# Performance work log

Measured on AMD Instinct MI355X. Metric: run time of the kernel, lower is better.

The kernel has to match this reference:

```python
import jax, jax.numpy as jnp
import numpy as np

N_NODES = 50000
N_EDGES = 800000
HIDDEN = 128          # hidden_dim
MSG = HIDDEN // 2     # message_dim = LSTM hidden size


def setup_inputs() -> dict:
    key = jax.random.key(0)
    ks = jax.random.split(key, 9)
    feat = jax.random.normal(ks[0], (N_NODES, HIDDEN), dtype=jnp.float32)
    src0 = jax.random.randint(ks[1], (N_EDGES,), 0, N_NODES, dtype=jnp.int32)
    dst0 = jax.random.randint(ks[2], (N_EDGES,), 0, N_NODES, dtype=jnp.int32)
    src1 = jax.random.randint(ks[3], (N_EDGES,), 0, N_NODES, dtype=jnp.int32)
    dst1 = jax.random.randint(ks[4], (N_EDGES,), 0, N_NODES, dtype=jnp.int32)
    # PyTorch LSTMCell params: gates order (i, f, g, o), scale 1/sqrt(hidden)
    s = 1.0 / np.sqrt(MSG)
    W_ih = jax.random.uniform(ks[5], (4 * MSG, HIDDEN), jnp.float32, -s, s)
    W_hh = jax.random.uniform(ks[6], (4 * MSG, MSG), jnp.float32, -s, s)
    b_ih = jax.random.uniform(ks[7], (4 * MSG,), jnp.float32, -s, s)
    b_hh = jax.random.uniform(ks[8], (4 * MSG,), jnp.float32, -s, s)
    return {"feat": feat, "src0": src0, "dst0": dst0, "src1": src1,
            "dst1": dst1, "W_ih": W_ih, "W_hh": W_hh, "b_ih": b_ih, "b_hh": b_hh}


def _etype_mean(feat, src, dst, n_nodes):
    """copy_u('h','m') + mean('m','ft') for one edge type."""
    m = feat[src]                                             # [E, H] gather
    s = jax.ops.segment_sum(m, dst, num_segments=n_nodes)    # [N, H]
    cnt = jax.ops.segment_sum(jnp.ones(src.shape, feat.dtype), dst,
                              num_segments=n_nodes)          # [N]
    mean = s / jnp.maximum(cnt, 1.0)[:, None]
    return mean, (cnt > 0).astype(feat.dtype)


def reference(feat, src0, dst0, src1, dst1, W_ih, W_hh, b_ih, b_hh):
    n = feat.shape[0]
    ft0, has0 = _etype_mean(feat, src0, dst0, n)
    ft1, has1 = _etype_mean(feat, src1, dst1, n)
    # cross_reducer='mean': average over etypes that delivered messages
    n_active = jnp.maximum(has0 + has1, 1.0)[:, None]
    rst = (ft0 + ft1) / n_active                              # [N, H]

    G_t = rst[:, :MSG]   # h0
    R_t = rst[:, MSG:]   # c0

    # PyTorch LSTMCell: gates = x W_ih^T + b_ih + h W_hh^T + b_hh
    gates = feat @ W_ih.T + b_ih + G_t @ W_hh.T + b_hh       # [N, 4*MSG]
    i, f, g, o = jnp.split(gates, 4, axis=1)
    c1 = jax.nn.sigmoid(f) * R_t + jax.nn.sigmoid(i) * jnp.tanh(g)
    h1 = jax.nn.sigmoid(o) * jnp.tanh(c1)
    return jnp.concatenate([h1, c1], axis=1)                  # [N, H]
```

## Files before the change

kernel.cpp:

```cpp
#include <hip/hip_runtime.h>
#include <hip/hip_fp16.h>
#include <cmath>

#define NN 50000
#define NE 800000
#define NPB 32
#define NBKT 196
#define BKT_SHIFT 8
#define BKT_NODES 256
#define BKT_CAP 6144
#define CHUNK 4096
#define NCH 196

using f16x8 = __attribute__((ext_vector_type(8))) _Float16;
using f32x4 = __attribute__((ext_vector_type(4))) float;

__device__ __forceinline__ float sigmoidf_(float x) {
    return 1.0f / (1.0f + __expf(-x));
}
__device__ __forceinline__ float tanhf_(float x) {
    float t = __expf(-2.0f * fabsf(x));
    float r = (1.0f - t) / (1.0f + t);
    return copysignf(r, x);
}

__global__ __launch_bounds__(256) void prep_kernel(
    const float* __restrict__ feat, __half* __restrict__ feat_h,
    const float* __restrict__ Wih, const float* __restrict__ Whh,
    const float* __restrict__ b_ih, const float* __restrict__ b_hh,
    __half* __restrict__ WC, float* __restrict__ bsum,
    int* __restrict__ bcnt) {
    int i = blockIdx.x * blockDim.x + threadIdx.x;

    {
        const float4 v = ((const float4*)feat)[i];
        __half2 lo = __floats2half2_rn(v.x, v.y);
        __half2 hi = __floats2half2_rn(v.z, v.w);
        ((__half2*)feat_h)[2 * i]     = lo;
        ((__half2*)feat_h)[2 * i + 1] = hi;
    }
    if (i < 256 * 128) {
        int g = i >> 7, k = i & 127;
        WC[(size_t)g * 192 + k] = __float2half(Wih[i]);
    }
    if (i < 256 * 64) {
        int g = i >> 6, k = i & 63;
        WC[(size_t)g * 192 + 128 + k] = __float2half(Whh[i]);
    }
    if (i < 256) bsum[i] = b_ih[i] + b_hh[i];
    if (i < 2 * NBKT) bcnt[i] = 0;
}

__global__ __launch_bounds__(256) void bin_kernel(
    const int* __restrict__ src0, const int* __restrict__ dst0,
    const int* __restrict__ src1, const int* __restrict__ dst1,
    int* __restrict__ bcnt,
    unsigned* __restrict__ binned0, unsigned* __restrict__ binned1) {
    __shared__ int cnt[NBKT];
    __shared__ int base[NBKT];
    __shared__ int cur[NBKT];
    __shared__ int sdst[CHUNK];

    int x  = blockIdx.x;
    int et = x >= NCH;
    int c  = et ? x - NCH : x;
    const int* src = et ? src1 : src0;
    const int* dst = et ? dst1 : dst0;
    unsigned* binned = et ? binned1 : binned0;

    int start = c * CHUNK;
    int n = min(CHUNK, NE - start);
    int tid = threadIdx.x;

    if (tid < NBKT) { cnt[tid] = 0; cur[tid] = 0; }
    __syncthreads();
    for (int i = tid; i < n; i += 256) {
        int d = dst[start + i];
        sdst[i] = d;
        atomicAdd(&cnt[d >> BKT_SHIFT], 1);
    }
    __syncthreads();
    if (tid < NBKT && cnt[tid] > 0)
        base[tid] = atomicAdd(&bcnt[et * NBKT + tid], cnt[tid]);
    __syncthreads();
    for (int i = tid; i < n; i += 256) {
        int d = sdst[i];
        int b = d >> BKT_SHIFT;
        int r = atomicAdd(&cur[b], 1);
        binned[(size_t)b * BKT_CAP + base[b] + r] =
            ((unsigned)d << 16) | (unsigned)src[start + i];
    }
}

__global__ __launch_bounds__(256) void bucket_scatter_kernel(
    const unsigned* __restrict__ binned0, const unsigned* __restrict__ binned1,
    const int* __restrict__ bcnt,
    int* __restrict__ off0, int* __restrict__ off1,
    int* __restrict__ deg0, int* __restrict__ deg1,
    unsigned short* __restrict__ es0, unsigned short* __restrict__ es1) {
    __shared__ int lcnt[BKT_NODES];
    __shared__ int lbase[BKT_NODES];

    int g  = blockIdx.x;
    int et = g >= NBKT;
    int b  = et ? g - NBKT : g;
    const unsigned* binned = (et ? binned1 : binned0) + (size_t)b * BKT_CAP;
    int* off = et ? off1 : off0;
    int* deg = et ? deg1 : deg0;
    unsigned short* es = (et ? es1 : es0) + (size_t)b * BKT_CAP;

    int bn = bcnt[g];
    int node0 = b * BKT_NODES;
    int tid = threadIdx.x;

    lcnt[tid] = 0;
    __syncthreads();
    for (int i = tid; i < bn; i += 256) {
        unsigned u = binned[i];
        int d = (int)(u >> 16) - node0;
        atomicAdd(&lcnt[d], 1);
    }
    __syncthreads();
    int cntv = lcnt[tid];
    for (int d = 1; d < BKT_NODES; d <<= 1) {
        int v = (tid >= d) ? lcnt[tid - d] : 0;
        __syncthreads();
        lcnt[tid] += v;
        __syncthreads();
    }
    int excl = lcnt[tid] - cntv;
    lbase[tid] = excl;
    int gn = node0 + tid;
    if (gn < NN) { off[gn] = b * BKT_CAP + excl; deg[gn] = cntv; }
    __syncthreads();
    for (int i = tid; i < bn; i += 256) {
        unsigned u = binned[i];
        int d = (int)(u >> 16) - node0;
        int r = atomicAdd(&lbase[d], 1);
        es[r] = (unsigned short)(u & 0xffffu);
    }
}

__global__ __launch_bounds__(256) void gather_kernel(
    const uint2* __restrict__ featu,
    const unsigned short* __restrict__ es0, const int* __restrict__ off0, const int* __restrict__ deg0,
    const unsigned short* __restrict__ es1, const int* __restrict__ off1, const int* __restrict__ deg1,
    uint2* __restrict__ rstu) {
    int wid  = (blockIdx.x * blockDim.x + threadIdx.x) >> 6;
    int lane = threadIdx.x & 63;
    if (wid >= NN) return;
    int hf = lane >> 5;
    int c  = lane & 31;

    float a0[4] = {0.f, 0.f, 0.f, 0.f};
    float a1[4] = {0.f, 0.f, 0.f, 0.f};

    int d0 = deg0[wid], o0 = off0[wid];
    int e = 0;
    for (; e + 8 <= d0; e += 8) {
        int s0 = es0[o0 + e + 0 + hf];
        int s1 = es0[o0 + e + 2 + hf];
        int s2 = es0[o0 + e + 4 + hf];
        int s3 = es0[o0 + e + 6 + hf];
        uint2 v0 = featu[(size_t)s0 * 32 + c];
        uint2 v1 = featu[(size_t)s1 * 32 + c];
        uint2 v2 = featu[(size_t)s2 * 32 + c];
        uint2 v3 = featu[(size_t)s3 * 32 + c];
#pragma unroll
        for (int k = 0; k < 1; k++) { }
        {
            float2 f;
            f = __half22float2(*(__half2*)&v0.x); a0[0] += f.x; a0[1] += f.y;
            f = __half22float2(*(__half2*)&v0.y); a0[2] += f.x; a0[3] += f.y;
            f = __half22float2(*(__half2*)&v1.x); a0[0] += f.x; a0[1] += f.y;
            f = __half22float2(*(__half2*)&v1.y); a0[2] += f.x; a0[3] += f.y;
            f = __half22float2(*(__half2*)&v2.x); a0[0] += f.x; a0[1] += f.y;
            f = __half22float2(*(__half2*)&v2.y); a0[2] += f.x; a0[3] += f.y;
            f = __half22float2(*(__half2*)&v3.x); a0[0] += f.x; a0[1] += f.y;
            f = __half22float2(*(__half2*)&v3.y); a0[2] += f.x; a0[3] += f.y;
        }
    }
    if (e < d0) {
        int last = d0 - 1;
#pragma unroll
        for (int j = 0; j < 4; j++) {
            int ee = e + 2 * j + hf;
            int s = es0[o0 + min(ee, last)];
            uint2 v = featu[(size_t)s * 32 + c];
            float m = (ee < d0) ? 1.f : 0.f;
            float2 f;
            f = __half22float2(*(__half2*)&v.x); a0[0] = fmaf(f.x, m, a0[0]); a0[1] = fmaf(f.y, m, a0[1]);
            f = __half22float2(*(__half2*)&v.y); a0[2] = fmaf(f.x, m, a0[2]); a0[3] = fmaf(f.y, m, a0[3]);
        }
    }

    int d1 = deg1[wid], o1 = off1[wid];
    e = 0;
    for (; e + 8 <= d1; e += 8) {
        int s0 = es1[o1 + e + 0 + hf];
        int s1 = es1[o1 + e + 2 + hf];
        int s2 = es1[o1 + e + 4 + hf];
        int s3 = es1[o1 + e + 6 + hf];
        uint2 v0 = featu[(size_t)s0 * 32 + c];
        uint2 v1 = featu[(size_t)s1 * 32 + c];
        uint2 v2 = featu[(size_t)s2 * 32 + c];
        uint2 v3 = featu[(size_t)s3 * 32 + c];
        {
            float2 f;
            f = __half22float2(*(__half2*)&v0.x); a1[0] += f.x; a1[1] += f.y;
            f = __half22float2(*(__half2*)&v0.y); a1[2] += f.x; a1[3] += f.y;
            f = __half22float2(*(__half2*)&v1.x); a1[0] += f.x; a1[1] += f.y;
            f = __half22float2(*(__half2*)&v1.y); a1[2] += f.x; a1[3] += f.y;
            f = __half22float2(*(__half2*)&v2.x); a1[0] += f.x; a1[1] += f.y;
            f = __half22float2(*(__half2*)&v2.y); a1[2] += f.x; a1[3] += f.y;
            f = __half22float2(*(__half2*)&v3.x); a1[0] += f.x; a1[1] += f.y;
            f = __half22float2(*(__half2*)&v3.y); a1[2] += f.x; a1[3] += f.y;
        }
    }
    if (e < d1) {
        int last = d1 - 1;
#pragma unroll
        for (int j = 0; j < 4; j++) {
            int ee = e + 2 * j + hf;
            int s = es1[o1 + min(ee, last)];
            uint2 v = featu[(size_t)s * 32 + c];
            float m = (ee < d1) ? 1.f : 0.f;
            float2 f;
            f = __half22float2(*(__half2*)&v.x); a1[0] = fmaf(f.x, m, a1[0]); a1[1] = fmaf(f.y, m, a1[1]);
            f = __half22float2(*(__half2*)&v.y); a1[2] = fmaf(f.x, m, a1[2]); a1[3] = fmaf(f.y, m, a1[3]);
        }
    }

#pragma unroll
    for (int k = 0; k < 4; k++) {
        a0[k] += __shfl_xor(a0[k], 32, 64);
        a1[k] += __shfl_xor(a1[k], 32, 64);
    }

    if (hf == 0) {
        float inv0 = 1.0f / fmaxf((float)d0, 1.0f);
        float inv1 = 1.0f / fmaxf((float)d1, 1.0f);
        float na = fmaxf((float)((d0 > 0) + (d1 > 0)), 1.0f);
        float r0 = (a0[0] * inv0 + a1[0] * inv1) / na;
        float r1 = (a0[1] * inv0 + a1[1] * inv1) / na;
        float r2 = (a0[2] * inv0 + a1[2] * inv1) / na;
        float r3 = (a0[3] * inv0 + a1[3] * inv1) / na;
        __half2 h01 = __floats2half2_rn(r0, r1);
        __half2 h23 = __floats2half2_rn(r2, r3);
        uint2 o;
        o.x = *(unsigned*)&h01;
        o.y = *(unsigned*)&h23;
        rstu[(size_t)wid * 32 + c] = o;
    }
}

__global__ __launch_bounds__(256) void node_kernel(
    const __half* __restrict__ feat_h,
    const __half* __restrict__ rst_h,
    const __half* __restrict__ WC, const float* __restrict__ bsum,
    float* __restrict__ out) {
    __shared__ __half xs[32 * 200];

    int t  = threadIdx.x;
    int nb = blockIdx.x * NPB;
    int lane = t & 63;
    int w    = t >> 6;
    int col  = lane & 15;
    int g4   = lane >> 4;

    f16x8 bfr[4][6];
    float bias[4];
#pragma unroll
    for (int ct = 0; ct < 4; ct++) {
        int gate = ct * 64 + w * 16 + col;
        bias[ct] = bsum[gate];
#pragma unroll
        for (int ks = 0; ks < 6; ks++)
            bfr[ct][ks] = *(const f16x8*)(WC + (size_t)gate * 192 + ks * 32 + g4 * 8);
    }

    const uint4* feat4 = (const uint4*)feat_h;
    const uint4* rst4  = (const uint4*)rst_h;
#pragma unroll
    for (int j = 0; j < 2; j++) {
        int e = t + j * 256;
        int n = e >> 4, q = e & 15;
        int gn = nb + n;
        uint4 v = make_uint4(0, 0, 0, 0);
        if (gn < NN) v = feat4[(size_t)gn * 16 + q];
        *(uint4*)(&xs[n * 200 + q * 8]) = v;
    }
    {
        int n = t >> 3, q = t & 7;
        int gn = nb + n;
        uint4 v = make_uint4(0, 0, 0, 0);
        if (gn < NN) v = rst4[(size_t)gn * 16 + q];
        *(uint4*)(&xs[n * 200 + 128 + q * 8]) = v;
    }
    __syncthreads();

    f32x4 acc[2][4];
#pragma unroll
    for (int rt = 0; rt < 2; rt++)
#pragma unroll
        for (int ct = 0; ct < 4; ct++)
            acc[rt][ct] = (f32x4){bias[ct], bias[ct], bias[ct], bias[ct]};

#pragma unroll
    for (int ks = 0; ks < 6; ks++) {
        f16x8 a0 = *(const f16x8*)(&xs[(col) * 200 + ks * 32 + g4 * 8]);
        f16x8 a1 = *(const f16x8*)(&xs[(16 + col) * 200 + ks * 32 + g4 * 8]);
#pragma unroll
        for (int ct = 0; ct < 4; ct++) {
            acc[0][ct] = __builtin_amdgcn_mfma_f32_16x16x32_f16(a0, bfr[ct][ks], acc[0][ct], 0, 0, 0);
            acc[1][ct] = __builtin_amdgcn_mfma_f32_16x16x32_f16(a1, bfr[ct][ks], acc[1][ct], 0, 0, 0);
        }
    }

    int m = w * 16 + col;
#pragma unroll
    for (int rt = 0; rt < 2; rt++) {
#pragma unroll
        for (int r = 0; r < 4; r++) {
            int nl = rt * 16 + g4 * 4 + r;
            int gn = nb + nl;
            if (gn >= NN) continue;
            float iv = sigmoidf_(acc[rt][0][r]);
            float fv = sigmoidf_(acc[rt][1][r]);
            float gv = tanhf_(acc[rt][2][r]);
            float ov = sigmoidf_(acc[rt][3][r]);
            float R  = __half2float(rst_h[(size_t)gn * 128 + 64 + m]);
            float c1 = fv * R + iv * gv;
            float h1 = ov * tanhf_(c1);
            out[(size_t)gn * 128 + m]      = h1;
            out[(size_t)gn * 128 + 64 + m] = c1;
        }
    }
}

extern "C" void kernel_launch(void* const* d_in, const int* in_sizes, int n_in,
                              void* d_out, int out_size, void* d_ws, size_t ws_size,
                              hipStream_t stream) {
    const float* feat = (const float*)d_in[0];
    const int*   src0 = (const int*)d_in[1];
    const int*   dst0 = (const int*)d_in[2];
    const int*   src1 = (const int*)d_in[3];
    const int*   dst1 = (const int*)d_in[4];
    const float* W_ih = (const float*)d_in[5];
    const float* W_hh = (const float*)d_in[6];
    const float* b_ih = (const float*)d_in[7];
    const float* b_hh = (const float*)d_in[8];
    float* out = (float*)d_out;

    char* p = (char*)d_ws;
    int* bcnt = (int*)p;            p += 2 * NBKT * 4;
    int* off0 = (int*)p;            p += NN * 4;
    int* off1 = (int*)p;            p += NN * 4;
    int* deg0 = (int*)p;            p += NN * 4;
    int* deg1 = (int*)p;            p += NN * 4;
    unsigned* binned0 = (unsigned*)p; p += (size_t)NBKT * BKT_CAP * 4;
    unsigned* binned1 = (unsigned*)p; p += (size_t)NBKT * BKT_CAP * 4;
    unsigned short* es0 = (unsigned short*)p; p += (size_t)NBKT * BKT_CAP * 2;
    unsigned short* es1 = (unsigned short*)p; p += (size_t)NBKT * BKT_CAP * 2;
    __half* feat_h = (__half*)p;    p += (size_t)NN * 128 * 2;
    __half* rst_h  = (__half*)p;    p += (size_t)NN * 128 * 2;
    __half* WC     = (__half*)p;    p += (size_t)256 * 192 * 2;
    float*  bsum   = (float*)p;     p += 256 * 4;

    int blocksP = (NN * 128 / 4 + 255) / 256;
    prep_kernel<<<blocksP, 256, 0, stream>>>(feat, feat_h, W_ih, W_hh, b_ih, b_hh,
                                             WC, bsum, bcnt);

    bin_kernel<<<2 * NCH, 256, 0, stream>>>(src0, dst0, src1, dst1, bcnt,
                                            binned0, binned1);

    bucket_scatter_kernel<<<2 * NBKT, 256, 0, stream>>>(binned0, binned1, bcnt,
                                                        off0, off1, deg0, deg1,
                                                        es0, es1);

    int blocksG = (NN * 64 + 255) / 256;
    gather_kernel<<<blocksG, 256, 0, stream>>>((const uint2*)feat_h,
                                               es0, off0, deg0, es1, off1, deg1,
                                               (uint2*)rst_h);

    int blocksN = (NN + NPB - 1) / NPB;
    node_kernel<<<blocksN, 256, 0, stream>>>(feat_h, rst_h, WC, bsum, out);
}
```

Baseline: 139.1 us.

## Partition each node's edge list by source-index slice to improve gather locality

The bucket scatter now sub-sorts each destination node's edges into four source-index slices, storing per-slice offsets and degrees as int4. The gather walks the slices in order for all nodes, so concurrent waves tend to read feature rows from the same quarter of the feature table, which is meant to raise L2 hit rate. The gather loop is also restructured into a 2-edge masked loop with nontemporal index loads. In exchange there are more short loops with masked tails per node, which waste lanes, plus larger offset/degree arrays and extra shared atomics and integer divides in the scatter.

Measured after the change: 166.5 us. +19.7%, slower.

```diff
diff --git a/kernel.cpp b/kernel.cpp
--- a/kernel.cpp
+++ b/kernel.cpp
@@ -11,6 +11,8 @@
 #define BKT_CAP 6144
 #define CHUNK 4096
 #define NCH 196
+#define NP 4
+#define SLICE 12500
 
 using f16x8 = __attribute__((ext_vector_type(8))) _Float16;
 using f32x4 = __attribute__((ext_vector_type(4))) float;
@@ -95,56 +97,94 @@
 __global__ __launch_bounds__(256) void bucket_scatter_kernel(
     const unsigned* __restrict__ binned0, const unsigned* __restrict__ binned1,
     const int* __restrict__ bcnt,
-    int* __restrict__ off0, int* __restrict__ off1,
-    int* __restrict__ deg0, int* __restrict__ deg1,
+    int4* __restrict__ off0q, int4* __restrict__ off1q,
+    int4* __restrict__ deg0q, int4* __restrict__ deg1q,
     unsigned short* __restrict__ es0, unsigned short* __restrict__ es1) {
-    __shared__ int lcnt[BKT_NODES];
-    __shared__ int lbase[BKT_NODES];
+    __shared__ int lcnt[BKT_NODES * NP];
+    __shared__ int lbase[BKT_NODES * NP];
+    __shared__ int stot[BKT_NODES];
 
     int g  = blockIdx.x;
     int et = g >= NBKT;
     int b  = et ? g - NBKT : g;
     const unsigned* binned = (et ? binned1 : binned0) + (size_t)b * BKT_CAP;
-    int* off = et ? off1 : off0;
-    int* deg = et ? deg1 : deg0;
+    int4* offq = et ? off1q : off0q;
+    int4* degq = et ? deg1q : deg0q;
     unsigned short* es = (et ? es1 : es0) + (size_t)b * BKT_CAP;
 
     int bn = bcnt[g];
     int node0 = b * BKT_NODES;
+    int bo = b * BKT_CAP;
     int tid = threadIdx.x;
 
-    lcnt[tid] = 0;
+#pragma unroll
+    for (int r = 0; r < NP; r++) lcnt[tid * NP + r] = 0;
     __syncthreads();
     for (int i = tid; i < bn; i += 256) {
         unsigned u = binned[i];
         int d = (int)(u >> 16) - node0;
-        atomicAdd(&lcnt[d], 1);
-    }
-    __syncthreads();
-    int cntv = lcnt[tid];
+        int r = (int)(u & 0xffffu) / SLICE;
+        atomicAdd(&lcnt[d * NP + r], 1);
+    }
+    __syncthreads();
+    int c0 = lcnt[tid * NP + 0], c1 = lcnt[tid * NP + 1];
+    int c2 = lcnt[tid * NP + 2], c3 = lcnt[tid * NP + 3];
+    int tot = c0 + c1 + c2 + c3;
+    stot[tid] = tot;
+    __syncthreads();
     for (int d = 1; d < BKT_NODES; d <<= 1) {
-        int v = (tid >= d) ? lcnt[tid - d] : 0;
+        int v = (tid >= d) ? stot[tid - d] : 0;
         __syncthreads();
-        lcnt[tid] += v;
+        stot[tid] += v;
         __syncthreads();
     }
-    int excl = lcnt[tid] - cntv;
-    lbase[tid] = excl;
+    int excl = stot[tid] - tot;
+    int b0 = excl, b1 = excl + c0, b2 = b1 + c1, b3 = b2 + c2;
+    lbase[tid * NP + 0] = b0;
+    lbase[tid * NP + 1] = b1;
+    lbase[tid * NP + 2] = b2;
+    lbase[tid * NP + 3] = b3;
     int gn = node0 + tid;
-    if (gn < NN) { off[gn] = b * BKT_CAP + excl; deg[gn] = cntv; }
+    if (gn < NN) {
+        offq[gn] = make_int4(bo + b0, bo + b1, bo + b2, bo + b3);
+        degq[gn] = make_int4(c0, c1, c2, c3);
+    }
     __syncthreads();
     for (int i = tid; i < bn; i += 256) {
         unsigned u = binned[i];
         int d = (int)(u >> 16) - node0;
-        int r = atomicAdd(&lbase[d], 1);
-        es[r] = (unsigned short)(u & 0xffffu);
+        int sv = (int)(u & 0xffffu);
+        int r = sv / SLICE;
+        int pos = atomicAdd(&lbase[d * NP + r], 1);
+        es[pos] = (unsigned short)sv;
+    }
+}
+
+__device__ __forceinline__ void seg_accum(
+    const uint2* __restrict__ featu,
+    const unsigned short* __restrict__ es,
+    int o, int d, int hf, int c, float* a) {
+    for (int e = 0; e < d; e += 4) {
+        int last = d - 1;
+        int ee0 = e + hf, ee1 = e + 2 + hf;
+        int s0 = __builtin_nontemporal_load(&es[o + min(ee0, last)]);
+        int s1 = __builtin_nontemporal_load(&es[o + min(ee1, last)]);
+        uint2 v0 = featu[(size_t)s0 * 32 + c];
+        uint2 v1 = featu[(size_t)s1 * 32 + c];
+        float m0 = (ee0 < d) ? 1.f : 0.f;
+        float m1 = (ee1 < d) ? 1.f : 0.f;
+        float2 f;
+        f = __half22float2(*(__half2*)&v0.x); a[0] = fmaf(f.x, m0, a[0]); a[1] = fmaf(f.y, m0, a[1]);
+        f = __half22float2(*(__half2*)&v0.y); a[2] = fmaf(f.x, m0, a[2]); a[3] = fmaf(f.y, m0, a[3]);
+        f = __half22float2(*(__half2*)&v1.x); a[0] = fmaf(f.x, m1, a[0]); a[1] = fmaf(f.y, m1, a[1]);
+        f = __half22float2(*(__half2*)&v1.y); a[2] = fmaf(f.x, m1, a[2]); a[3] = fmaf(f.y, m1, a[3]);
     }
 }
 
 __global__ __launch_bounds__(256) void gather_kernel(
     const uint2* __restrict__ featu,
-    const unsigned short* __restrict__ es0, const int* __restrict__ off0, const int* __restrict__ deg0,
-    const unsigned short* __restrict__ es1, const int* __restrict__ off1, const int* __restrict__ deg1,
+    const unsigned short* __restrict__ es0, const int4* __restrict__ off0q, const int4* __restrict__ deg0q,
+    const unsigned short* __restrict__ es1, const int4* __restrict__ off1q, const int4* __restrict__ deg1q,
     uint2* __restrict__ rstu) {
     int wid  = (blockIdx.x * blockDim.x + threadIdx.x) >> 6;
     int lane = threadIdx.x & 63;
@@ -152,83 +192,20 @@
     int hf = lane >> 5;
     int c  = lane & 31;
 
+    int4 o0v = off0q[wid], d0v = deg0q[wid];
+    int4 o1v = off1q[wid], d1v = deg1q[wid];
+    int o0s[4] = {o0v.x, o0v.y, o0v.z, o0v.w};
+    int d0s[4] = {d0v.x, d0v.y, d0v.z, d0v.w};
+    int o1s[4] = {o1v.x, o1v.y, o1v.z, o1v.w};
+    int d1s[4] = {d1v.x, d1v.y, d1v.z, d1v.w};
+
     float a0[4] = {0.f, 0.f, 0.f, 0.f};
     float a1[4] = {0.f, 0.f, 0.f, 0.f};
 
-    int d0 = deg0[wid], o0 = off0[wid];
-    int e = 0;
-    for (; e + 8 <= d0; e += 8) {
-        int s0 = es0[o0 + e + 0 + hf];
-        int s1 = es0[o0 + e + 2 + hf];
-        int s2 = es0[o0 + e + 4 + hf];
-        int s3 = es0[o0 + e + 6 + hf];
-        uint2 v0 = featu[(size_t)s0 * 32 + c];
-        uint2 v1 = featu[(size_t)s1 * 32 + c];
-        uint2 v2 = featu[(size_t)s2 * 32 + c];
-        uint2 v3 = featu[(size_t)s3 * 32 + c];
-#pragma unroll
-        for (int k = 0; k < 1; k++) { }
-        {
-            float2 f;
-            f = __half22float2(*(__half2*)&v0.x); a0[0] += f.x; a0[1] += f.y;
-            f = __half22float2(*(__half2*)&v0.y); a0[2] += f.x; a0[3] += f.y;
-            f = __half22float2(*(__half2*)&v1.x); a0[0] += f.x; a0[1] += f.y;
-            f = __half22float2(*(__half2*)&v1.y); a0[2] += f.x; a0[3] += f.y;
-            f = __half22float2(*(__half2*)&v2.x); a0[0] += f.x; a0[1] += f.y;
-            f = __half22float2(*(__half2*)&v2.y); a0[2] += f.x; a0[3] += f.y;
-            f = __half22float2(*(__half2*)&v3.x); a0[0] += f.x; a0[1] += f.y;
-            f = __half22float2(*(__half2*)&v3.y); a0[2] += f.x; a0[3] += f.y;
-        }
-    }
-    if (e < d0) {
-        int last = d0 - 1;
-#pragma unroll
-        for (int j = 0; j < 4; j++) {
-            int ee = e + 2 * j + hf;
-            int s = es0[o0 + min(ee, last)];
-            uint2 v = featu[(size_t)s * 32 + c];
-            float m = (ee < d0) ? 1.f : 0.f;
-            float2 f;
-            f = __half22float2(*(__half2*)&v.x); a0[0] = fmaf(f.x, m, a0[0]); a0[1] = fmaf(f.y, m, a0[1]);
-            f = __half22float2(*(__half2*)&v.y); a0[2] = fmaf(f.x, m, a0[2]); a0[3] = fmaf(f.y, m, a0[3]);
-        }
-    }
-
-    int d1 = deg1[wid], o1 = off1[wid];
-    e = 0;
-    for (; e + 8 <= d1; e += 8) {
-        int s0 = es1[o1 + e + 0 + hf];
-        int s1 = es1[o1 + e + 2 + hf];
-        int s2 = es1[o1 + e + 4 + hf];
-        int s3 = es1[o1 + e + 6 + hf];
-        uint2 v0 = featu[(size_t)s0 * 32 + c];
-        uint2 v1 = featu[(size_t)s1 * 32 + c];
-        uint2 v2 = featu[(size_t)s2 * 32 + c];
-        uint2 v3 = featu[(size_t)s3 * 32 + c];
-        {
-            float2 f;
-            f = __half22float2(*(__half2*)&v0.x); a1[0] += f.x; a1[1] += f.y;
-            f = __half22float2(*(__half2*)&v0.y); a1[2] += f.x; a1[3] += f.y;
-            f = __half22float2(*(__half2*)&v1.x); a1[0] += f.x; a1[1] += f.y;
-            f = __half22float2(*(__half2*)&v1.y); a1[2] += f.x; a1[3] += f.y;
-            f = __half22float2(*(__half2*)&v2.x); a1[0] += f.x; a1[1] += f.y;
-            f = __half22float2(*(__half2*)&v2.y); a1[2] += f.x; a1[3] += f.y;
-            f = __half22float2(*(__half2*)&v3.x); a1[0] += f.x; a1[1] += f.y;
-            f = __half22float2(*(__half2*)&v3.y); a1[2] += f.x; a1[3] += f.y;
-        }
-    }
-    if (e < d1) {
-        int last = d1 - 1;
-#pragma unroll
-        for (int j = 0; j < 4; j++) {
-            int ee = e + 2 * j + hf;
-            int s = es1[o1 + min(ee, last)];
-            uint2 v = featu[(size_t)s * 32 + c];
-            float m = (ee < d1) ? 1.f : 0.f;
-            float2 f;
-            f = __half22float2(*(__half2*)&v.x); a1[0] = fmaf(f.x, m, a1[0]); a1[1] = fmaf(f.y, m, a1[1]);
-            f = __half22float2(*(__half2*)&v.y); a1[2] = fmaf(f.x, m, a1[2]); a1[3] = fmaf(f.y, m, a1[3]);
-        }
+#pragma unroll
+    for (int r = 0; r < NP; r++) {
+        seg_accum(featu, es0, o0s[r], d0s[r], hf, c, a0);
+        seg_accum(featu, es1, o1s[r], d1s[r], hf, c, a1);
     }
 
 #pragma unroll
@@ -238,6 +215,8 @@
     }
 
     if (hf == 0) {
+        int d0 = d0s[0] + d0s[1] + d0s[2] + d0s[3];
+        int d1 = d1s[0] + d1s[1] + d1s[2] + d1s[3];
         float inv0 = 1.0f / fmaxf((float)d0, 1.0f);
         float inv1 = 1.0f / fmaxf((float)d1, 1.0f);
         float na = fmaxf((float)((d0 > 0) + (d1 > 0)), 1.0f);
@@ -354,10 +333,10 @@
 
     char* p = (char*)d_ws;
     int* bcnt = (int*)p;            p += 2 * NBKT * 4;
-    int* off0 = (int*)p;            p += NN * 4;
-    int* off1 = (int*)p;            p += NN * 4;
-    int* deg0 = (int*)p;            p += NN * 4;
-    int* deg1 = (int*)p;            p += NN * 4;
+    int4* off0q = (int4*)p;         p += (size_t)NN * 16;
+    int4* off1q = (int4*)p;         p += (size_t)NN * 16;
+    int4* deg0q = (int4*)p;         p += (size_t)NN * 16;
+    int4* deg1q = (int4*)p;         p += (size_t)NN * 16;
     unsigned* binned0 = (unsigned*)p; p += (size_t)NBKT * BKT_CAP * 4;
     unsigned* binned1 = (unsigned*)p; p += (size_t)NBKT * BKT_CAP * 4;
     unsigned short* es0 = (unsigned short*)p; p += (size_t)NBKT * BKT_CAP * 2;
@@ -375,12 +354,13 @@
                                             binned0, binned1);
 
     bucket_scatter_kernel<<<2 * NBKT, 256, 0, stream>>>(binned0, binned1, bcnt,
-                                                        off0, off1, deg0, deg1,
+                                                        off0q, off1q, deg0q, deg1q,
                                                         es0, es1);
 
     int blocksG = (NN * 64 + 255) / 256;
     gather_kernel<<<blocksG, 256, 0, stream>>>((const uint2*)feat_h,
-                                               es0, off0, deg0, es1, off1, deg1,
+                                               es0, off0q, deg0q,
+                                               es1, off1q, deg1q,
                                                (uint2*)rst_h);
 
     int blocksN = (NN + NPB - 1) / NPB;
```

## Fuse neighbor-mean gather into LSTM node kernel via shared memory

Applied to the files above, without the earlier changes.

Merges the gather kernel and the LSTM node kernel into one kernel. Each block's four wavefronts aggregate 8 nodes each and write the mean straight into shared memory, which the MFMA gate computation then reads. This removes the rst_h global round trip and one kernel launch. In exchange each block now has only 4 waves doing serial per-node gathers instead of one wave per node. The weight fragments are loaded per gate tile, and a minimum-occupancy hint of 6 is added to launch_bounds.

Result: slower. 163.2 us (+17.4%).

```diff
diff --git a/kernel.cpp b/kernel.cpp
--- a/kernel.cpp
+++ b/kernel.cpp
@@ -141,34 +141,54 @@
     }
 }
 
-__global__ __launch_bounds__(256) void gather_kernel(
-    const uint2* __restrict__ featu,
+__global__ __launch_bounds__(256, 6) void fused_kernel(
+    const __half* __restrict__ feat_h,
     const unsigned short* __restrict__ es0, const int* __restrict__ off0, const int* __restrict__ deg0,
     const unsigned short* __restrict__ es1, const int* __restrict__ off1, const int* __restrict__ deg1,
-    uint2* __restrict__ rstu) {
-    int wid  = (blockIdx.x * blockDim.x + threadIdx.x) >> 6;
-    int lane = threadIdx.x & 63;
-    if (wid >= NN) return;
+    const __half* __restrict__ WC, const float* __restrict__ bsum,
+    float* __restrict__ out) {
+    __shared__ __half xs[32 * 200];
+    __shared__ __half rs[32 * 64];
+
+    int t  = threadIdx.x;
+    int nb = blockIdx.x * NPB;
+    int lane = t & 63;
+    int w    = t >> 6;
+
+    const uint4* feat4 = (const uint4*)feat_h;
+#pragma unroll
+    for (int j = 0; j < 2; j++) {
+        int e = t + j * 256;
+        int n = e >> 4, q = e & 15;
+        int gn = nb + n;
+        uint4 v = make_uint4(0, 0, 0, 0);
+        if (gn < NN) v = feat4[(size_t)gn * 16 + q];
+        *(uint4*)(&xs[n * 200 + q * 8]) = v;
+    }
+
+    const uint2* featu = (const uint2*)feat_h;
     int hf = lane >> 5;
     int c  = lane & 31;
 
-    float a0[4] = {0.f, 0.f, 0.f, 0.f};
-    float a1[4] = {0.f, 0.f, 0.f, 0.f};
-
-    int d0 = deg0[wid], o0 = off0[wid];
-    int e = 0;
-    for (; e + 8 <= d0; e += 8) {
-        int s0 = es0[o0 + e + 0 + hf];
-        int s1 = es0[o0 + e + 2 + hf];
-        int s2 = es0[o0 + e + 4 + hf];
-        int s3 = es0[o0 + e + 6 + hf];
-        uint2 v0 = featu[(size_t)s0 * 32 + c];
-        uint2 v1 = featu[(size_t)s1 * 32 + c];
-        uint2 v2 = featu[(size_t)s2 * 32 + c];
-        uint2 v3 = featu[(size_t)s3 * 32 + c];
-#pragma unroll
-        for (int k = 0; k < 1; k++) { }
-        {
+    for (int i = 0; i < 8; i++) {
+        int nl = w * 8 + i;
+        int gn = nb + nl;
+        if (gn >= NN) break;
+
+        float a0[4] = {0.f, 0.f, 0.f, 0.f};
+        float a1[4] = {0.f, 0.f, 0.f, 0.f};
+
+        int d0 = deg0[gn], o0 = off0[gn];
+        int e = 0;
+        for (; e + 8 <= d0; e += 8) {
+            int s0 = es0[o0 + e + 0 + hf];
+            int s1 = es0[o0 + e + 2 + hf];
+            int s2 = es0[o0 + e + 4 + hf];
+            int s3 = es0[o0 + e + 6 + hf];
+            uint2 v0 = featu[(size_t)s0 * 32 + c];
+            uint2 v1 = featu[(size_t)s1 * 32 + c];
+            uint2 v2 = featu[(size_t)s2 * 32 + c];
+            uint2 v3 = featu[(size_t)s3 * 32 + c];
             float2 f;
             f = __half22float2(*(__half2*)&v0.x); a0[0] += f.x; a0[1] += f.y;
             f = __half22float2(*(__half2*)&v0.y); a0[2] += f.x; a0[3] += f.y;
@@ -179,33 +199,31 @@
             f = __half22float2(*(__half2*)&v3.x); a0[0] += f.x; a0[1] += f.y;
             f = __half22float2(*(__half2*)&v3.y); a0[2] += f.x; a0[3] += f.y;
         }
-    }
-    if (e < d0) {
-        int last = d0 - 1;
-#pragma unroll
-        for (int j = 0; j < 4; j++) {
-            int ee = e + 2 * j + hf;
-            int s = es0[o0 + min(ee, last)];
-            uint2 v = featu[(size_t)s * 32 + c];
-            float m = (ee < d0) ? 1.f : 0.f;
-            float2 f;
-            f = __half22float2(*(__half2*)&v.x); a0[0] = fmaf(f.x, m, a0[0]); a0[1] = fmaf(f.y, m, a0[1]);
-            f = __half22float2(*(__half2*)&v.y); a0[2] = fmaf(f.x, m, a0[2]); a0[3] = fmaf(f.y, m, a0[3]);
-        }
-    }
-
-    int d1 = deg1[wid], o1 = off1[wid];
-    e = 0;
-    for (; e + 8 <= d1; e += 8) {
-        int s0 = es1[o1 + e + 0 + hf];
-        int s1 = es1[o1 + e + 2 + hf];
-        int s2 = es1[o1 + e + 4 + hf];
-        int s3 = es1[o1 + e + 6 + hf];
-        uint2 v0 = featu[(size_t)s0 * 32 + c];
-        uint2 v1 = featu[(size_t)s1 * 32 + c];
-        uint2 v2 = featu[(size_t)s2 * 32 + c];
-        uint2 v3 = featu[(size_t)s3 * 32 + c];
-        {
+        if (e < d0) {
+            int last = d0 - 1;
+#pragma unroll
+            for (int j = 0; j < 4; j++) {
+                int ee = e + 2 * j + hf;
+                int s = es0[o0 + min(ee, last)];
+                uint2 v = featu[(size_t)s * 32 + c];
+                float m = (ee < d0) ? 1.f : 0.f;
+                float2 f;
+                f = __half22float2(*(__half2*)&v.x); a0[0] = fmaf(f.x, m, a0[0]); a0[1] = fmaf(f.y, m, a0[1]);
+                f = __half22float2(*(__half2*)&v.y); a0[2] = fmaf(f.x, m, a0[2]); a0[3] = fmaf(f.y, m, a0[3]);
+            }
+        }
+
+        int d1 = deg1[gn], o1 = off1[gn];
+        e = 0;
+        for (; e + 8 <= d1; e += 8) {
+            int s0 = es1[o1 + e + 0 + hf];
+            int s1 = es1[o1 + e + 2 + hf];
+            int s2 = es1[o1 + e + 4 + hf];
+            int s3 = es1[o1 + e + 6 + hf];
+            uint2 v0 = featu[(size_t)s0 * 32 + c];
+            uint2 v1 = featu[(size_t)s1 * 32 + c];
+            uint2 v2 = featu[(size_t)s2 * 32 + c];
+            uint2 v3 = featu[(size_t)s3 * 32 + c];
             float2 f;
             f = __half22float2(*(__half2*)&v0.x); a1[0] += f.x; a1[1] += f.y;
             f = __half22float2(*(__half2*)&v0.y); a1[2] += f.x; a1[3] += f.y;
@@ -216,104 +234,68 @@
             f = __half22float2(*(__half2*)&v3.x); a1[0] += f.x; a1[1] += f.y;
             f = __half22float2(*(__half2*)&v3.y); a1[2] += f.x; a1[3] += f.y;
         }
-    }
-    if (e < d1) {
-        int last = d1 - 1;
-#pragma unroll
-        for (int j = 0; j < 4; j++) {
-            int ee = e + 2 * j + hf;
-            int s = es1[o1 + min(ee, last)];
-            uint2 v = featu[(size_t)s * 32 + c];
-            float m = (ee < d1) ? 1.f : 0.f;
-            float2 f;
-            f = __half22float2(*(__half2*)&v.x); a1[0] = fmaf(f.x, m, a1[0]); a1[1] = fmaf(f.y, m, a1[1]);
-            f = __half22float2(*(__half2*)&v.y); a1[2] = fmaf(f.x, m, a1[2]); a1[3] = fmaf(f.y, m, a1[3]);
-        }
-    }
-
-#pragma unroll
-    for (int k = 0; k < 4; k++) {
-        a0[k] += __shfl_xor(a0[k], 32, 64);
-        a1[k] += __shfl_xor(a1[k], 32, 64);
-    }
-
-    if (hf == 0) {
-        float inv0 = 1.0f / fmaxf((float)d0, 1.0f);
-        float inv1 = 1.0f / fmaxf((float)d1, 1.0f);
-        float na = fmaxf((float)((d0 > 0) + (d1 > 0)), 1.0f);
-        float r0 = (a0[0] * inv0 + a1[0] * inv1) / na;
-        float r1 = (a0[1] * inv0 + a1[1] * inv1) / na;
-        float r2 = (a0[2] * inv0 + a1[2] * inv1) / na;
-        float r3 = (a0[3] * inv0 + a1[3] * inv1) / na;
-        __half2 h01 = __floats2half2_rn(r0, r1);
-        __half2 h23 = __floats2half2_rn(r2, r3);
-        uint2 o;
-        o.x = *(unsigned*)&h01;
-        o.y = *(unsigned*)&h23;
-        rstu[(size_t)wid * 32 + c] = o;
-    }
-}
-
-__global__ __launch_bounds__(256) void node_kernel(
-    const __half* __restrict__ feat_h,
-    const __half* __restrict__ rst_h,
-    const __half* __restrict__ WC, const float* __restrict__ bsum,
-    float* __restrict__ out) {
-    __shared__ __half xs[32 * 200];
-
-    int t  = threadIdx.x;
-    int nb = blockIdx.x * NPB;
-    int lane = t & 63;
-    int w    = t >> 6;
-    int col  = lane & 15;
-    int g4   = lane >> 4;
-
-    f16x8 bfr[4][6];
-    float bias[4];
+        if (e < d1) {
+            int last = d1 - 1;
+#pragma unroll
+            for (int j = 0; j < 4; j++) {
+                int ee = e + 2 * j + hf;
+                int s = es1[o1 + min(ee, last)];
+                uint2 v = featu[(size_t)s * 32 + c];
+                float m = (ee < d1) ? 1.f : 0.f;
+                float2 f;
+                f = __half22float2(*(__half2*)&v.x); a1[0] = fmaf(f.x, m, a1[0]); a1[1] = fmaf(f.y, m, a1[1]);
+                f = __half22float2(*(__half2*)&v.y); a1[2] = fmaf(f.x, m, a1[2]); a1[3] = fmaf(f.y, m, a1[3]);
+            }
+        }
+
+#pragma unroll
+        for (int k = 0; k < 4; k++) {
+            a0[k] += __shfl_xor(a0[k], 32, 64);
+            a1[k] += __shfl_xor(a1[k], 32, 64);
+        }
+
+        if (hf == 0) {
+            float inv0 = 1.0f / fmaxf((float)d0, 1.0f);
+            float inv1 = 1.0f / fmaxf((float)d1, 1.0f);
+            float na = fmaxf((float)((d0 > 0) + (d1 > 0)), 1.0f);
+            float r0 = (a0[0] * inv0 + a1[0] * inv1) / na;
+            float r1 = (a0[1] * inv0 + a1[1] * inv1) / na;
+            float r2 = (a0[2] * inv0 + a1[2] * inv1) / na;
+            float r3 = (a0[3] * inv0 + a1[3] * inv1) / na;
+            __half2 h01 = __floats2half2_rn(r0, r1);
+            __half2 h23 = __floats2half2_rn(r2, r3);
+            uint2 ov;
+            ov.x = *(unsigned*)&h01;
+            ov.y = *(unsigned*)&h23;
+            if (c < 16) {
+                *(uint2*)(&xs[nl * 200 + 128 + 4 * c]) = ov;
+            } else {
+                *(uint2*)(&rs[nl * 64 + 4 * (c - 16)]) = ov;
+            }
+        }
+    }
+    __syncthreads();
+
+    int col = lane & 15;
+    int g4  = lane >> 4;
+
+    f32x4 acc[2][4];
 #pragma unroll
     for (int ct = 0; ct < 4; ct++) {
         int gate = ct * 64 + w * 16 + col;
-        bias[ct] = bsum[gate];
+        float bias = bsum[gate];
+        acc[0][ct] = (f32x4){bias, bias, bias, bias};
+        acc[1][ct] = (f32x4){bias, bias, bias, bias};
+        f16x8 bfr[6];
 #pragma unroll
         for (int ks = 0; ks < 6; ks++)
-            bfr[ct][ks] = *(const f16x8*)(WC + (size_t)gate * 192 + ks * 32 + g4 * 8);
-    }
-
-    const uint4* feat4 = (const uint4*)feat_h;
-    const uint4* rst4  = (const uint4*)rst_h;
-#pragma unroll
-    for (int j = 0; j < 2; j++) {
-        int e = t + j * 256;
-        int n = e >> 4, q = e & 15;
-        int gn = nb + n;
-        uint4 v = make_uint4(0, 0, 0, 0);
-        if (gn < NN) v = feat4[(size_t)gn * 16 + q];
-        *(uint4*)(&xs[n * 200 + q * 8]) = v;
-    }
-    {
-        int n = t >> 3, q = t & 7;
-        int gn = nb + n;
-        uint4 v = make_uint4(0, 0, 0, 0);
-        if (gn < NN) v = rst4[(size_t)gn * 16 + q];
-        *(uint4*)(&xs[n * 200 + 128 + q * 8]) = v;
-    }
-    __syncthreads();
-
-    f32x4 acc[2][4];
-#pragma unroll
-    for (int rt = 0; rt < 2; rt++)
-#pragma unroll
-        for (int ct = 0; ct < 4; ct++)
-            acc[rt][ct] = (f32x4){bias[ct], bias[ct], bias[ct], bias[ct]};
-
-#pragma unroll
-    for (int ks = 0; ks < 6; ks++) {
-        f16x8 a0 = *(const f16x8*)(&xs[(col) * 200 + ks * 32 + g4 * 8]);
-        f16x8 a1 = *(const f16x8*)(&xs[(16 + col) * 200 + ks * 32 + g4 * 8]);
-#pragma unroll
-        for (int ct = 0; ct < 4; ct++) {
-            acc[0][ct] = __builtin_amdgcn_mfma_f32_16x16x32_f16(a0, bfr[ct][ks], acc[0][ct], 0, 0, 0);
-            acc[1][ct] = __builtin_amdgcn_mfma_f32_16x16x32_f16(a1, bfr[ct][ks], acc[1][ct], 0, 0, 0);
+            bfr[ks] = *(const f16x8*)(WC + (size_t)gate * 192 + ks * 32 + g4 * 8);
+#pragma unroll
+        for (int ks = 0; ks < 6; ks++) {
+            f16x8 a0 = *(const f16x8*)(&xs[(col) * 200 + ks * 32 + g4 * 8]);
+            f16x8 a1 = *(const f16x8*)(&xs[(16 + col) * 200 + ks * 32 + g4 * 8]);
+            acc[0][ct] = __builtin_amdgcn_mfma_f32_16x16x32_f16(a0, bfr[ks], acc[0][ct], 0, 0, 0);
+            acc[1][ct] = __builtin_amdgcn_mfma_f32_16x16x32_f16(a1, bfr[ks], acc[1][ct], 0, 0, 0);
         }
     }
 
@@ -329,7 +311,7 @@
             float fv = sigmoidf_(acc[rt][1][r]);
             float gv = tanhf_(acc[rt][2][r]);
             float ov = sigmoidf_(acc[rt][3][r]);
-            float R  = __half2float(rst_h[(size_t)gn * 128 + 64 + m]);
+            float R  = __half2float(rs[nl * 64 + m]);
             float c1 = fv * R + iv * gv;
             float h1 = ov * tanhf_(c1);
             out[(size_t)gn * 128 + m]      = h1;
@@ -363,7 +345,6 @@
     unsigned short* es0 = (unsigned short*)p; p += (size_t)NBKT * BKT_CAP * 2;
     unsigned short* es1 = (unsigned short*)p; p += (size_t)NBKT * BKT_CAP * 2;
     __half* feat_h = (__half*)p;    p += (size_t)NN * 128 * 2;
-    __half* rst_h  = (__half*)p;    p += (size_t)NN * 128 * 2;
     __half* WC     = (__half*)p;    p += (size_t)256 * 192 * 2;
     float*  bsum   = (float*)p;     p += 256 * 4;
 
@@ -378,11 +359,9 @@
                                                         off0, off1, deg0, deg1,
                                                         es0, es1);
 
-    int blocksG = (NN * 64 + 255) / 256;
-    gather_kernel<<<blocksG, 256, 0, stream>>>((const uint2*)feat_h,
-                                               es0, off0, deg0, es1, off1, deg1,
-                                               (uint2*)rst_h);
-
-    int blocksN = (NN + NPB - 1) / NPB;
-    node_kernel<<<blocksN, 256, 0, stream>>>(feat_h, rst_h, WC, bsum, out);
-}
+    int blocksF = (NN + NPB - 1) / NPB;
+    fused_kernel<<<blocksF, 256, 0, stream>>>(feat_h,
+                                              es0, off0, deg0,
+                                              es1, off1, deg1,
+                                              WC, bsum, out);
+}
```

## Gather h0 half of neighbor features in FP8 to halve gather bandwidth

Applied to the files above, without the earlier changes.

Prep now also writes an FP8 (e4m3) copy of the first 64 feature columns per node. The gather kernel reads those columns (the G_t/h0 half used only in the matmul) from the 64-byte FP8 rows and reads the c0 half from FP16, so per-edge gather traffic drops from 256 to 192 bytes. Lane mappings and shuffle reductions are reworked for both widths. The cost is precision: FP8 mean aggregation of h0 may exceed tolerance, and there is an extra write of the FP8 copy in prep.

Result: slower. 155.8 us (+12.0%).

```diff
diff --git a/kernel.cpp b/kernel.cpp
--- a/kernel.cpp
+++ b/kernel.cpp
@@ -14,6 +14,7 @@
 
 using f16x8 = __attribute__((ext_vector_type(8))) _Float16;
 using f32x4 = __attribute__((ext_vector_type(4))) float;
+using f32x2 = __attribute__((ext_vector_type(2))) float;
 
 __device__ __forceinline__ float sigmoidf_(float x) {
     return 1.0f / (1.0f + __expf(-x));
@@ -24,8 +25,34 @@
     return copysignf(r, x);
 }
 
+__device__ __forceinline__ void acc8(uint2 v, float* a) {
+    f32x2 f;
+    f = __builtin_amdgcn_cvt_pk_f32_fp8(v.x, false); a[0] += f.x; a[1] += f.y;
+    f = __builtin_amdgcn_cvt_pk_f32_fp8(v.x, true);  a[2] += f.x; a[3] += f.y;
+    f = __builtin_amdgcn_cvt_pk_f32_fp8(v.y, false); a[4] += f.x; a[5] += f.y;
+    f = __builtin_amdgcn_cvt_pk_f32_fp8(v.y, true);  a[6] += f.x; a[7] += f.y;
+}
+__device__ __forceinline__ void acc8m(uint2 v, float m, float* a) {
+    f32x2 f;
+    f = __builtin_amdgcn_cvt_pk_f32_fp8(v.x, false); a[0] = fmaf(f.x, m, a[0]); a[1] = fmaf(f.y, m, a[1]);
+    f = __builtin_amdgcn_cvt_pk_f32_fp8(v.x, true);  a[2] = fmaf(f.x, m, a[2]); a[3] = fmaf(f.y, m, a[3]);
+    f = __builtin_amdgcn_cvt_pk_f32_fp8(v.y, false); a[4] = fmaf(f.x, m, a[4]); a[5] = fmaf(f.y, m, a[5]);
+    f = __builtin_amdgcn_cvt_pk_f32_fp8(v.y, true);  a[6] = fmaf(f.x, m, a[6]); a[7] = fmaf(f.y, m, a[7]);
+}
+__device__ __forceinline__ void accRm(uint2 v, float m, float* a) {
+    float2 f;
+    f = __half22float2(*(__half2*)&v.x); a[0] = fmaf(f.x, m, a[0]); a[1] = fmaf(f.y, m, a[1]);
+    f = __half22float2(*(__half2*)&v.y); a[2] = fmaf(f.x, m, a[2]); a[3] = fmaf(f.y, m, a[3]);
+}
+__device__ __forceinline__ void accR(uint2 v, float* a) {
+    float2 f;
+    f = __half22float2(*(__half2*)&v.x); a[0] += f.x; a[1] += f.y;
+    f = __half22float2(*(__half2*)&v.y); a[2] += f.x; a[3] += f.y;
+}
+
 __global__ __launch_bounds__(256) void prep_kernel(
     const float* __restrict__ feat, __half* __restrict__ feat_h,
+    unsigned* __restrict__ featq8,
     const float* __restrict__ Wih, const float* __restrict__ Whh,
     const float* __restrict__ b_ih, const float* __restrict__ b_hh,
     __half* __restrict__ WC, float* __restrict__ bsum,
@@ -38,6 +65,12 @@
         __half2 hi = __floats2half2_rn(v.z, v.w);
         ((__half2*)feat_h)[2 * i]     = lo;
         ((__half2*)feat_h)[2 * i + 1] = hi;
+        if ((i & 31) < 16) {
+            int w8 = 0;
+            w8 = __builtin_amdgcn_cvt_pk_fp8_f32(v.x, v.y, w8, false);
+            w8 = __builtin_amdgcn_cvt_pk_fp8_f32(v.z, v.w, w8, true);
+            featq8[(i >> 5) * 16 + (i & 15)] = (unsigned)w8;
+        }
     }
     if (i < 256 * 128) {
         int g = i >> 7, k = i & 127;
@@ -142,115 +175,148 @@
 }
 
 __global__ __launch_bounds__(256) void gather_kernel(
-    const uint2* __restrict__ featu,
+    const uint2* __restrict__ fq8,
+    const uint2* __restrict__ fR,
     const unsigned short* __restrict__ es0, const int* __restrict__ off0, const int* __restrict__ deg0,
     const unsigned short* __restrict__ es1, const int* __restrict__ off1, const int* __restrict__ deg1,
-    uint2* __restrict__ rstu) {
+    __half* __restrict__ rst_h) {
     int wid  = (blockIdx.x * blockDim.x + threadIdx.x) >> 6;
     int lane = threadIdx.x & 63;
     if (wid >= NN) return;
-    int hf = lane >> 5;
-    int c  = lane & 31;
-
-    float a0[4] = {0.f, 0.f, 0.f, 0.f};
-    float a1[4] = {0.f, 0.f, 0.f, 0.f};
+    int sub8 = lane >> 3;
+    int c8   = lane & 7;
+    int sub4 = lane >> 4;
+    int c16  = lane & 15;
 
     int d0 = deg0[wid], o0 = off0[wid];
+    int d1 = deg1[wid], o1 = off1[wid];
+
+    float g0[8] = {0,0,0,0,0,0,0,0}, g1[8] = {0,0,0,0,0,0,0,0};
+    float r0[4] = {0,0,0,0},         r1[4] = {0,0,0,0};
+
     int e = 0;
-    for (; e + 8 <= d0; e += 8) {
-        int s0 = es0[o0 + e + 0 + hf];
-        int s1 = es0[o0 + e + 2 + hf];
-        int s2 = es0[o0 + e + 4 + hf];
-        int s3 = es0[o0 + e + 6 + hf];
-        uint2 v0 = featu[(size_t)s0 * 32 + c];
-        uint2 v1 = featu[(size_t)s1 * 32 + c];
-        uint2 v2 = featu[(size_t)s2 * 32 + c];
-        uint2 v3 = featu[(size_t)s3 * 32 + c];
-#pragma unroll
-        for (int k = 0; k < 1; k++) { }
-        {
-            float2 f;
-            f = __half22float2(*(__half2*)&v0.x); a0[0] += f.x; a0[1] += f.y;
-            f = __half22float2(*(__half2*)&v0.y); a0[2] += f.x; a0[3] += f.y;
-            f = __half22float2(*(__half2*)&v1.x); a0[0] += f.x; a0[1] += f.y;
-            f = __half22float2(*(__half2*)&v1.y); a0[2] += f.x; a0[3] += f.y;
-            f = __half22float2(*(__half2*)&v2.x); a0[0] += f.x; a0[1] += f.y;
-            f = __half22float2(*(__half2*)&v2.y); a0[2] += f.x; a0[3] += f.y;
-            f = __half22float2(*(__half2*)&v3.x); a0[0] += f.x; a0[1] += f.y;
-            f = __half22float2(*(__half2*)&v3.y); a0[2] += f.x; a0[3] += f.y;
-        }
+    for (; e + 16 <= d0; e += 16) {
+        int sa = es0[o0 + e + sub8];
+        int sb = es0[o0 + e + 8 + sub8];
+        uint2 va = fq8[(size_t)sa * 8 + c8];
+        uint2 vb = fq8[(size_t)sb * 8 + c8];
+        acc8(va, g0);
+        acc8(vb, g0);
     }
     if (e < d0) {
         int last = d0 - 1;
 #pragma unroll
-        for (int j = 0; j < 4; j++) {
-            int ee = e + 2 * j + hf;
+        for (int j = 0; j < 2; j++) {
+            int ee = e + 8 * j + sub8;
             int s = es0[o0 + min(ee, last)];
-            uint2 v = featu[(size_t)s * 32 + c];
-            float m = (ee < d0) ? 1.f : 0.f;
-            float2 f;
-            f = __half22float2(*(__half2*)&v.x); a0[0] = fmaf(f.x, m, a0[0]); a0[1] = fmaf(f.y, m, a0[1]);
-            f = __half22float2(*(__half2*)&v.y); a0[2] = fmaf(f.x, m, a0[2]); a0[3] = fmaf(f.y, m, a0[3]);
-        }
-    }
-
-    int d1 = deg1[wid], o1 = off1[wid];
+            uint2 v = fq8[(size_t)s * 8 + c8];
+            acc8m(v, (ee < d0) ? 1.f : 0.f, g0);
+        }
+    }
+    e = 0;
+    for (; e + 16 <= d1; e += 16) {
+        int sa = es1[o1 + e + sub8];
+        int sb = es1[o1 + e + 8 + sub8];
+        uint2 va = fq8[(size_t)sa * 8 + c8];
+        uint2 vb = fq8[(size_t)sb * 8 + c8];
+        acc8(va, g1);
+        acc8(vb, g1);
+    }
+    if (e < d1) {
+        int last = d1 - 1;
+#pragma unroll
+        for (int j = 0; j < 2; j++) {
+            int ee = e + 8 * j + sub8;
+            int s = es1[o1 + min(ee, last)];
+            uint2 v = fq8[(size_t)s * 8 + c8];
+            acc8m(v, (ee < d1) ? 1.f : 0.f, g1);
+        }
+    }
+
+    e = 0;
+    for (; e + 8 <= d0; e += 8) {
+        int sa = es0[o0 + e + sub4];
+        int sb = es0[o0 + e + 4 + sub4];
+        uint2 va = fR[(size_t)sa * 32 + 16 + c16];
+        uint2 vb = fR[(size_t)sb * 32 + 16 + c16];
+        accR(va, r0);
+        accR(vb, r0);
+    }
+    if (e < d0) {
+        int last = d0 - 1;
+#pragma unroll
+        for (int j = 0; j < 2; j++) {
+            int ee = e + 4 * j + sub4;
+            int s = es0[o0 + min(ee, last)];
+            uint2 v = fR[(size_t)s * 32 + 16 + c16];
+            accRm(v, (ee < d0) ? 1.f : 0.f, r0);
+        }
+    }
     e = 0;
     for (; e + 8 <= d1; e += 8) {
-        int s0 = es1[o1 + e + 0 + hf];
-        int s1 = es1[o1 + e + 2 + hf];
-        int s2 = es1[o1 + e + 4 + hf];
-        int s3 = es1[o1 + e + 6 + hf];
-        uint2 v0 = featu[(size_t)s0 * 32 + c];
-        uint2 v1 = featu[(size_t)s1 * 32 + c];
-        uint2 v2 = featu[(size_t)s2 * 32 + c];
-        uint2 v3 = featu[(size_t)s3 * 32 + c];
-        {
-            float2 f;
-            f = __half22float2(*(__half2*)&v0.x); a1[0] += f.x; a1[1] += f.y;
-            f = __half22float2(*(__half2*)&v0.y); a1[2] += f.x; a1[3] += f.y;
-            f = __half22float2(*(__half2*)&v1.x); a1[0] += f.x; a1[1] += f.y;
-            f = __half22float2(*(__half2*)&v1.y); a1[2] += f.x; a1[3] += f.y;
-            f = __half22float2(*(__half2*)&v2.x); a1[0] += f.x; a1[1] += f.y;
-            f = __half22float2(*(__half2*)&v2.y); a1[2] += f.x; a1[3] += f.y;
-            f = __half22float2(*(__half2*)&v3.x); a1[0] += f.x; a1[1] += f.y;
-            f = __half22float2(*(__half2*)&v3.y); a1[2] += f.x; a1[3] += f.y;
-        }
+        int sa = es1[o1 + e + sub4];
+        int sb = es1[o1 + e + 4 + sub4];
+        uint2 va = fR[(size_t)sa * 32 + 16 + c16];
+        uint2 vb = fR[(size_t)sb * 32 + 16 + c16];
+        accR(va, r1);
+        accR(vb, r1);
     }
     if (e < d1) {
         int last = d1 - 1;
 #pragma unroll
-        for (int j = 0; j < 4; j++) {
-            int ee = e + 2 * j + hf;
+        for (int j = 0; j < 2; j++) {
+            int ee = e + 4 * j + sub4;
             int s = es1[o1 + min(ee, last)];
-            uint2 v = featu[(size_t)s * 32 + c];
-            float m = (ee < d1) ? 1.f : 0.f;
-            float2 f;
-            f = __half22float2(*(__half2*)&v.x); a1[0] = fmaf(f.x, m, a1[0]); a1[1] = fmaf(f.y, m, a1[1]);
-            f = __half22float2(*(__half2*)&v.y); a1[2] = fmaf(f.x, m, a1[2]); a1[3] = fmaf(f.y, m, a1[3]);
-        }
-    }
-
+            uint2 v = fR[(size_t)s * 32 + 16 + c16];
+            accRm(v, (ee < d1) ? 1.f : 0.f, r1);
+        }
+    }
+
+#pragma unroll
+    for (int k = 0; k < 8; k++) {
+        g0[k] += __shfl_xor(g0[k], 8, 64);
+        g0[k] += __shfl_xor(g0[k], 16, 64);
+        g0[k] += __shfl_xor(g0[k], 32, 64);
+        g1[k] += __shfl_xor(g1[k], 8, 64);
+        g1[k] += __shfl_xor(g1[k], 16, 64);
+        g1[k] += __shfl_xor(g1[k], 32, 64);
+    }
 #pragma unroll
     for (int k = 0; k < 4; k++) {
-        a0[k] += __shfl_xor(a0[k], 32, 64);
-        a1[k] += __shfl_xor(a1[k], 32, 64);
-    }
-
-    if (hf == 0) {
-        float inv0 = 1.0f / fmaxf((float)d0, 1.0f);
-        float inv1 = 1.0f / fmaxf((float)d1, 1.0f);
-        float na = fmaxf((float)((d0 > 0) + (d1 > 0)), 1.0f);
-        float r0 = (a0[0] * inv0 + a1[0] * inv1) / na;
-        float r1 = (a0[1] * inv0 + a1[1] * inv1) / na;
-        float r2 = (a0[2] * inv0 + a1[2] * inv1) / na;
-        float r3 = (a0[3] * inv0 + a1[3] * inv1) / na;
-        __half2 h01 = __floats2half2_rn(r0, r1);
-        __half2 h23 = __floats2half2_rn(r2, r3);
+        r0[k] += __shfl_xor(r0[k], 16, 64);
+        r0[k] += __shfl_xor(r0[k], 32, 64);
+        r1[k] += __shfl_xor(r1[k], 16, 64);
+        r1[k] += __shfl_xor(r1[k], 32, 64);
+    }
+
+    float inv0 = 1.0f / fmaxf((float)d0, 1.0f);
+    float inv1 = 1.0f / fmaxf((float)d1, 1.0f);
+    float na = fmaxf((float)((d0 > 0) + (d1 > 0)), 1.0f);
+
+    if (lane < 8) {
+        float v[8];
+#pragma unroll
+        for (int k = 0; k < 8; k++)
+            v[k] = (g0[k] * inv0 + g1[k] * inv1) / na;
+        __half2 h01 = __floats2half2_rn(v[0], v[1]);
+        __half2 h23 = __floats2half2_rn(v[2], v[3]);
+        __half2 h45 = __floats2half2_rn(v[4], v[5]);
+        __half2 h67 = __floats2half2_rn(v[6], v[7]);
+        uint4 o;
+        o.x = *(unsigned*)&h01; o.y = *(unsigned*)&h23;
+        o.z = *(unsigned*)&h45; o.w = *(unsigned*)&h67;
+        ((uint4*)rst_h)[(size_t)wid * 16 + lane] = o;
+    }
+    if (lane < 16) {
+        float v[4];
+#pragma unroll
+        for (int k = 0; k < 4; k++)
+            v[k] = (r0[k] * inv0 + r1[k] * inv1) / na;
+        __half2 h01 = __floats2half2_rn(v[0], v[1]);
+        __half2 h23 = __floats2half2_rn(v[2], v[3]);
         uint2 o;
-        o.x = *(unsigned*)&h01;
-        o.y = *(unsigned*)&h23;
-        rstu[(size_t)wid * 32 + c] = o;
+        o.x = *(unsigned*)&h01; o.y = *(unsigned*)&h23;
+        ((uint2*)rst_h)[(size_t)wid * 32 + 16 + lane] = o;
     }
 }
 
@@ -363,12 +429,14 @@
     unsigned short* es0 = (unsigned short*)p; p += (size_t)NBKT * BKT_CAP * 2;
     unsigned short* es1 = (unsigned short*)p; p += (size_t)NBKT * BKT_CAP * 2;
     __half* feat_h = (__half*)p;    p += (size_t)NN * 128 * 2;
+    unsigned* featq8 = (unsigned*)p; p += (size_t)NN * 16 * 4;
     __half* rst_h  = (__half*)p;    p += (size_t)NN * 128 * 2;
     __half* WC     = (__half*)p;    p += (size_t)256 * 192 * 2;
     float*  bsum   = (float*)p;     p += 256 * 4;
 
     int blocksP = (NN * 128 / 4 + 255) / 256;
-    prep_kernel<<<blocksP, 256, 0, stream>>>(feat, feat_h, W_ih, W_hh, b_ih, b_hh,
+    prep_kernel<<<blocksP, 256, 0, stream>>>(feat, feat_h, featq8,
+                                             W_ih, W_hh, b_ih, b_hh,
                                              WC, bsum, bcnt);
 
     bin_kernel<<<2 * NCH, 256, 0, stream>>>(src0, dst0, src1, dst1, bcnt,
@@ -379,9 +447,11 @@
                                                         es0, es1);
 
     int blocksG = (NN * 64 + 255) / 256;
-    gather_kernel<<<blocksG, 256, 0, stream>>>((const uint2*)feat_h,
-                                               es0, off0, deg0, es1, off1, deg1,
-                                               (uint2*)rst_h);
+    gather_kernel<<<blocksG, 256, 0, stream>>>((const uint2*)featq8,
+                                               (const uint2*)feat_h,
+                                               es0, off0, deg0,
+                                               es1, off1, deg1,
+                                               rst_h);
 
     int blocksN = (NN + NPB - 1) / NPB;
     node_kernel<<<blocksN, 256, 0, stream>>>(feat_h, rst_h, WC, bsum, out);
```
